# Kernel optimization log

Hardware: AMD Instinct MI355X
Metric: run time of the kernel (lower is better)

## Reference

```python
import jax, jax.numpy as jnp
import numpy as np

N_NODES = 50000


def setup_inputs() -> dict:
    key = jax.random.key(0)
    k1, k2, k3, k4, k5, k6 = jax.random.split(key, 6)
    features = jax.random.normal(k1, (N_NODES, 128), dtype=jnp.float32)
    anchor_distances = jax.random.uniform(k2, (N_NODES, 64), dtype=jnp.float32)
    W = jax.random.normal(k3, (192, 128), dtype=jnp.float32) * (1.0 / np.sqrt(192.0))
    b = jax.random.normal(k4, (128,), dtype=jnp.float32) * 0.01
    src = jax.random.randint(k5, (800000,), 0, N_NODES, dtype=jnp.int32)
    dst = jax.random.randint(k6, (800000,), 0, N_NODES, dtype=jnp.int32)
    return {"features": features, "anchor_distances": anchor_distances,
            "W": W, "b": b, "src": src, "dst": dst}


def reference(features, anchor_distances, W, b, src, dst):
    # Linear(in_feats + num_anchors -> hidden) + ReLU
    combined = jnp.concatenate([features, anchor_distances], axis=1)  # [N, 192]
    h = jax.nn.relu(combined @ W + b)                                  # [N, H]
    # copy_u + mean aggregation: mean of h[src] grouped by dst
    msg_sum = jax.ops.segment_sum(h[src], dst, num_segments=N_NODES)  # [N, H]
    deg = jax.ops.segment_sum(jnp.ones_like(dst, dtype=h.dtype), dst,
                              num_segments=N_NODES)                    # [N]
    # DGL mean leaves 0 for isolated nodes; divide by max(deg, 1)
    out = msg_sum / jnp.maximum(deg, 1.0)[:, None]
    return out
```

## Files before the change

### kernel.cpp

```cpp
#include <hip/hip_runtime.h>
#include <hip/hip_bf16.h>


#define N_NODES 50000
#define N_EDGES 800000
#define HID 128
#define FDIM 128
#define ADIM 64
#define KDIM 192

#define BKT_SH 5
#define BKT_NODES 32
#define NBUCKETS ((N_NODES + BKT_NODES - 1) / BKT_NODES)
#define CAP 1024
#define PC_NBLK 256
#define PC_CHUNK ((N_EDGES + PC_NBLK - 1) / PC_NBLK)
#define EPT 13
#define GEMM_NBLK ((N_NODES + 31) / 32)
#define SA_LD 200

typedef __attribute__((ext_vector_type(8))) short short8;
typedef __attribute__((ext_vector_type(4))) float f32x4;
typedef __attribute__((ext_vector_type(4))) unsigned int u32x4;

__device__ inline unsigned short f2bf(float f) {
  unsigned u = __float_as_uint(f);
  u += 0x7FFFu + ((u >> 16) & 1u);
  return (unsigned short)(u >> 16);
}
__device__ inline unsigned pk2bf(float a, float b) {
  return (unsigned)f2bf(a) | ((unsigned)f2bf(b) << 16);
}
__device__ inline float bf2f(unsigned short s) {
  return __uint_as_float(((unsigned)s) << 16);
}

__global__ __launch_bounds__(256) void wbt_kernel(
    const float* __restrict__ W, unsigned short* __restrict__ WbTf,
    int* __restrict__ bcur) {
  if (blockIdx.x == 0) {
    for (int i = threadIdx.x; i < NBUCKETS; i += 256) bcur[i] = 0;
  }
  int idx = blockIdx.x * 256 + threadIdx.x;
  if (idx >= 2 * 4 * 6 * 64 * 8) return;
  int j = idx & 7;
  int lane = (idx >> 3) & 63;
  int frag = idx >> 9;
  int kk = frag % 6, p = frag / 6;
  int wn = p >> 2, nt = p & 3;
  int col = wn * 64 + nt * 16 + (lane & 15);
  int k = kk * 32 + (lane >> 4) * 8 + j;
  WbTf[idx] = f2bf(W[k * HID + col]);
}

#define SMEM_BYTES (32 * SA_LD * 2)
__global__ __launch_bounds__(256) void gemm_pscatter_kernel(
    const float* __restrict__ F, const float* __restrict__ A,
    const unsigned short* __restrict__ WbTf, const float* __restrict__ bias,
    unsigned short* __restrict__ hb,
    const int* __restrict__ src, const int* __restrict__ dst,
    int* __restrict__ bcur, unsigned* __restrict__ edata, int nrows) {
  __shared__ __align__(16) char smem_raw[SMEM_BYTES];

  if (blockIdx.x < PC_NBLK) {
    int* lh = (int*)smem_raw;
    int* lc = lh + NBUCKETS;
    int bp = blockIdx.x;
    for (int i = threadIdx.x; i < NBUCKETS; i += 256) lh[i] = 0;
    __syncthreads();
    int base = bp * PC_CHUNK;
    int end = base + PC_CHUNK; if (end > N_EDGES) end = N_EDGES;
    int rd[EPT], rs[EPT];
#pragma unroll
    for (int k = 0; k < EPT; ++k) {
      int j = base + threadIdx.x + k * 256;
      if (j < end) {
        rd[k] = dst[j];
        rs[k] = src[j];
        atomicAdd(&lh[rd[k] >> BKT_SH], 1);
      } else {
        rd[k] = -1;
      }
    }
    __syncthreads();
    for (int i = threadIdx.x; i < NBUCKETS; i += 256) {
      int c = lh[i];
      lh[i] = c ? atomicAdd(&bcur[i], c) : 0;
      lc[i] = 0;
    }
    __syncthreads();
#pragma unroll
    for (int k = 0; k < EPT; ++k) {
      if (rd[k] >= 0) {
        int bk = rd[k] >> BKT_SH, dl = rd[k] & (BKT_NODES - 1);
        int p = lh[bk] + atomicAdd(&lc[bk], 1);
        if (p < CAP)
          edata[(bk << 10) + p] = (unsigned)rs[k] | ((unsigned)dl << 16);
      }
    }
    return;
  }

  unsigned short* sA = (unsigned short*)smem_raw;
  const int gblk = blockIdx.x - PC_NBLK;
  const int tid = threadIdx.x;
  const int lane = tid & 63;
  const int wave = tid >> 6;
  const int wm = wave >> 1, wn = wave & 1;
  const int l15 = lane & 15, lg = lane >> 4;
  const int blockrow = gblk * 32;

#pragma unroll
  for (int it = 0; it < 4; ++it) {
    int i = tid + it * 256;
    int row = i >> 5, c4 = (i & 31) * 4;
    int crow = blockrow + row; crow = crow < nrows ? crow : (nrows - 1);
    float4 v = *(const float4*)(F + (size_t)crow * FDIM + c4);
    *(uint2*)(sA + row * SA_LD + c4) = make_uint2(pk2bf(v.x, v.y), pk2bf(v.z, v.w));
  }
#pragma unroll
  for (int it = 0; it < 2; ++it) {
    int i = tid + it * 256;
    int row = i >> 4, c4 = (i & 15) * 4;
    int crow = blockrow + row; crow = crow < nrows ? crow : (nrows - 1);
    float4 v = *(const float4*)(A + (size_t)crow * ADIM + c4);
    *(uint2*)(sA + row * SA_LD + FDIM + c4) = make_uint2(pk2bf(v.x, v.y), pk2bf(v.z, v.w));
  }

  short8 Bf[24];
#pragma unroll
  for (int nt = 0; nt < 4; ++nt)
#pragma unroll
    for (int kk = 0; kk < 6; ++kk)
      Bf[nt * 6 + kk] = *(const short8*)(
          WbTf + ((((wn * 4 + nt) * 6 + kk) << 9) + (lane << 3)));

  __syncthreads();

  short8 Af[6];
  const int rowl = wm * 16 + l15;
#pragma unroll
  for (int kk = 0; kk < 6; ++kk)
    Af[kk] = *(const short8*)(sA + rowl * SA_LD + kk * 32 + lg * 8);

  f32x4 acc[4] = {{0,0,0,0},{0,0,0,0},{0,0,0,0},{0,0,0,0}};
#pragma unroll
  for (int nt = 0; nt < 4; ++nt)
#pragma unroll
    for (int kk = 0; kk < 6; ++kk)
      acc[nt] = __builtin_amdgcn_mfma_f32_16x16x32_bf16(
          Af[kk], Bf[nt * 6 + kk], acc[nt], 0, 0, 0);

  const int rowbase = blockrow + wm * 16;
#pragma unroll
  for (int nt = 0; nt < 4; ++nt) {
    int col = wn * 64 + nt * 16 + l15;
    float bv = bias[col];
#pragma unroll
    for (int q = 0; q < 4; ++q) {
      int row = rowbase + lg * 4 + q;
      if (row < nrows) {
        float v = fmaxf(acc[nt][q] + bv, 0.f);
        hb[(size_t)row * HID + col] = f2bf(v);
      }
    }
  }
}

__device__ inline int wave_incl_scan(int v, int lane) {
#pragma unroll
  for (int off = 1; off < 64; off <<= 1) {
    int t = __shfl_up(v, off, 64);
    if (lane >= off) v += t;
  }
  return v;
}

#define EPT_A (CAP / 256)
__global__ __launch_bounds__(256) void bucket_agg_kernel(
    const unsigned short* __restrict__ hb, const int* __restrict__ bcur,
    const unsigned* __restrict__ edata, float* __restrict__ out) {
  int b = blockIdx.x;
  int nbase = b << BKT_SH;
  int nloc = N_NODES - nbase; if (nloc > BKT_NODES) nloc = BKT_NODES;
  int gb = b << 10;
  int cnt = bcur[b]; cnt = cnt < CAP ? cnt : CAP;
  int t = threadIdx.x, lane = t & 63, wave = t >> 6;
  int g = lane >> 4, l16 = lane & 15;

  __shared__ unsigned short ss[CAP];
  __shared__ int loff[BKT_NODES + 1];
  __shared__ int lcnt[BKT_NODES];
  __shared__ int lcur[BKT_NODES];

  unsigned er[EPT_A];
  if (t < BKT_NODES) lcnt[t] = 0;
  __syncthreads();
#pragma unroll
  for (int k = 0; k < EPT_A; ++k) {
    int j = t + k * 256;
    if (j < cnt) {
      er[k] = edata[gb + j];
      atomicAdd(&lcnt[er[k] >> 16], 1);
    } else {
      er[k] = 0xFFFFFFFFu;
    }
  }
  __syncthreads();
  if (wave == 0) {
    int v = (lane < BKT_NODES) ? lcnt[lane] : 0;
    int incl = wave_incl_scan(v, lane);
    if (lane < BKT_NODES) {
      loff[lane + 1] = incl;
      lcur[lane] = incl - v;
    }
    if (lane == 0) loff[0] = 0;
  }
  __syncthreads();
#pragma unroll
  for (int k = 0; k < EPT_A; ++k) {
    if (er[k] != 0xFFFFFFFFu) {
      int p = atomicAdd(&lcur[er[k] >> 16], 1);
      ss[p] = (unsigned short)(er[k] & 0xFFFFu);
    }
  }
  __syncthreads();
  const unsigned short* hbl = hb + l16 * 8;
  for (int n = wave; n < nloc; n += 4) {
    int s0 = loff[n], s1 = loff[n + 1];
    float acc[8] = {0, 0, 0, 0, 0, 0, 0, 0};
    int j = s0 + g;
    for (; j + 12 < s1; j += 16) {
      int e0 = ss[j], e1 = ss[j + 4], e2 = ss[j + 8], e3 = ss[j + 12];
      u32x4 v0 = *(const u32x4*)(hbl + (size_t)e0 * HID);
      u32x4 v1 = *(const u32x4*)(hbl + (size_t)e1 * HID);
      u32x4 v2 = *(const u32x4*)(hbl + (size_t)e2 * HID);
      u32x4 v3 = *(const u32x4*)(hbl + (size_t)e3 * HID);
#pragma unroll
      for (int i = 0; i < 4; ++i) {
        unsigned w0 = v0[i], w1 = v1[i], w2 = v2[i], w3 = v3[i];
        acc[2 * i]     += (bf2f((unsigned short)(w0 & 0xFFFFu))
                         + bf2f((unsigned short)(w1 & 0xFFFFu)))
                        + (bf2f((unsigned short)(w2 & 0xFFFFu))
                         + bf2f((unsigned short)(w3 & 0xFFFFu)));
        acc[2 * i + 1] += (bf2f((unsigned short)(w0 >> 16))
                         + bf2f((unsigned short)(w1 >> 16)))
                        + (bf2f((unsigned short)(w2 >> 16))
                         + bf2f((unsigned short)(w3 >> 16)));
      }
    }
    for (; j < s1; j += 4) {
      int e0 = ss[j];
      u32x4 v0 = *(const u32x4*)(hbl + (size_t)e0 * HID);
#pragma unroll
      for (int i = 0; i < 4; ++i) {
        unsigned w0 = v0[i];
        acc[2 * i]     += bf2f((unsigned short)(w0 & 0xFFFFu));
        acc[2 * i + 1] += bf2f((unsigned short)(w0 >> 16));
      }
    }
#pragma unroll
    for (int i = 0; i < 8; ++i) {
      acc[i] += __shfl_xor(acc[i], 16, 64);
      acc[i] += __shfl_xor(acc[i], 32, 64);
    }
    if (g == 0) {
      int d = s1 - s0;
      float inv = 1.0f / (float)(d > 1 ? d : 1);
      float* po = out + (size_t)(nbase + n) * HID + l16 * 8;
      *(float4*)po       = make_float4(acc[0]*inv, acc[1]*inv, acc[2]*inv, acc[3]*inv);
      *(float4*)(po + 4) = make_float4(acc[4]*inv, acc[5]*inv, acc[6]*inv, acc[7]*inv);
    }
  }
}

extern "C" void kernel_launch(void* const* d_in, const int* in_sizes, int n_in,
                              void* d_out, int out_size, void* d_ws, size_t ws_size,
                              hipStream_t stream) {
  const float* F   = (const float*)d_in[0];
  const float* A   = (const float*)d_in[1];
  const float* W   = (const float*)d_in[2];
  const float* b   = (const float*)d_in[3];
  const int*   src = (const int*)d_in[4];
  const int*   dst = (const int*)d_in[5];
  float* out = (float*)d_out;

  char* ws = (char*)d_ws;
  size_t off = 0;
  auto alloc = [&](size_t bytes) {
    char* p = ws + off;
    off += (bytes + 255) & ~(size_t)255;
    return p;
  };
  unsigned short* hb   = (unsigned short*)alloc((size_t)N_NODES * HID * 2);
  unsigned short* WbTf = (unsigned short*)alloc((size_t)HID * KDIM * 2);
  int* bcur = (int*)alloc((size_t)NBUCKETS * sizeof(int));
  unsigned* edata = (unsigned*)alloc((size_t)NBUCKETS * CAP * sizeof(unsigned));
  (void)ws_size;

  wbt_kernel<<<(KDIM * HID + 255) / 256, 256, 0, stream>>>(W, WbTf, bcur);
  gemm_pscatter_kernel<<<PC_NBLK + GEMM_NBLK, 256, 0, stream>>>(
      F, A, WbTf, b, hb, src, dst, bcur, edata, N_NODES);
  bucket_agg_kernel<<<NBUCKETS, 256, 0, stream>>>(hb, bcur, edata, out);
}
```

Measured before the change: 67.17 us.

## Replace bucketed edge partitioning with per-node global-atomic adjacency slots

Drops the two-level bucket partition (per-block shared histograms, bucket-offset atomics, and the in-kernel shared-memory counting sort in aggregation). Each edge now does one global atomicAdd on its destination's degree and writes its 16-bit source id into a fixed 64-slot per-node array. The edge scatter is merged into every GEMM block, and aggregation reads each node's slots directly, broadcasting indices with shuffles. This adds 800k contended global atomics and uncoalesced 2-byte writes, and silently drops edges beyond 64 per node. It also stores source ids as 16 bits although node ids reach 50000, which is fine only because that is below 65536.

```diff
diff --git a/kernel.cpp b/kernel.cpp
--- a/kernel.cpp
+++ b/kernel.cpp
@@ -9,14 +9,9 @@
 #define ADIM 64
 #define KDIM 192
 
-#define BKT_SH 5
-#define BKT_NODES 32
-#define NBUCKETS ((N_NODES + BKT_NODES - 1) / BKT_NODES)
-#define CAP 1024
-#define PC_NBLK 256
-#define PC_CHUNK ((N_EDGES + PC_NBLK - 1) / PC_NBLK)
-#define EPT 13
+#define DCAP 64
 #define GEMM_NBLK ((N_NODES + 31) / 32)
+#define EDGE_PER_BLK 512
 #define SA_LD 200
 
 typedef __attribute__((ext_vector_type(8))) short short8;
@@ -37,11 +32,9 @@
 
 __global__ __launch_bounds__(256) void wbt_kernel(
     const float* __restrict__ W, unsigned short* __restrict__ WbTf,
-    int* __restrict__ bcur) {
-  if (blockIdx.x == 0) {
-    for (int i = threadIdx.x; i < NBUCKETS; i += 256) bcur[i] = 0;
-  }
+    int* __restrict__ deg) {
   int idx = blockIdx.x * 256 + threadIdx.x;
+  if (idx < N_NODES) deg[idx] = 0;
   if (idx >= 2 * 4 * 6 * 64 * 8) return;
   int j = idx & 7;
   int lane = (idx >> 3) & 63;
@@ -59,56 +52,31 @@
     const unsigned short* __restrict__ WbTf, const float* __restrict__ bias,
     unsigned short* __restrict__ hb,
     const int* __restrict__ src, const int* __restrict__ dst,
-    int* __restrict__ bcur, unsigned* __restrict__ edata, int nrows) {
+    int* __restrict__ deg, unsigned short* __restrict__ edata, int nrows) {
   __shared__ __align__(16) char smem_raw[SMEM_BYTES];
-
-  if (blockIdx.x < PC_NBLK) {
-    int* lh = (int*)smem_raw;
-    int* lc = lh + NBUCKETS;
-    int bp = blockIdx.x;
-    for (int i = threadIdx.x; i < NBUCKETS; i += 256) lh[i] = 0;
-    __syncthreads();
-    int base = bp * PC_CHUNK;
-    int end = base + PC_CHUNK; if (end > N_EDGES) end = N_EDGES;
-    int rd[EPT], rs[EPT];
-#pragma unroll
-    for (int k = 0; k < EPT; ++k) {
-      int j = base + threadIdx.x + k * 256;
-      if (j < end) {
-        rd[k] = dst[j];
-        rs[k] = src[j];
-        atomicAdd(&lh[rd[k] >> BKT_SH], 1);
-      } else {
-        rd[k] = -1;
+  unsigned short* sA = (unsigned short*)smem_raw;
+  const int tid = threadIdx.x;
+
+  {
+    size_t ebase = (size_t)blockIdx.x * EDGE_PER_BLK + tid;
+#pragma unroll
+    for (int k = 0; k < 2; ++k) {
+      size_t e = ebase + (size_t)k * 256;
+      if (e < N_EDGES) {
+        int s = src[e];
+        int dnode = dst[e];
+        int p = atomicAdd(&deg[dnode], 1);
+        if (p < DCAP)
+          edata[(size_t)dnode * DCAP + p] = (unsigned short)s;
       }
     }
-    __syncthreads();
-    for (int i = threadIdx.x; i < NBUCKETS; i += 256) {
-      int c = lh[i];
-      lh[i] = c ? atomicAdd(&bcur[i], c) : 0;
-      lc[i] = 0;
-    }
-    __syncthreads();
-#pragma unroll
-    for (int k = 0; k < EPT; ++k) {
-      if (rd[k] >= 0) {
-        int bk = rd[k] >> BKT_SH, dl = rd[k] & (BKT_NODES - 1);
-        int p = lh[bk] + atomicAdd(&lc[bk], 1);
-        if (p < CAP)
-          edata[(bk << 10) + p] = (unsigned)rs[k] | ((unsigned)dl << 16);
-      }
-    }
-    return;
-  }
-
-  unsigned short* sA = (unsigned short*)smem_raw;
-  const int gblk = blockIdx.x - PC_NBLK;
-  const int tid = threadIdx.x;
+  }
+
   const int lane = tid & 63;
   const int wave = tid >> 6;
   const int wm = wave >> 1, wn = wave & 1;
   const int l15 = lane & 15, lg = lane >> 4;
-  const int blockrow = gblk * 32;
+  const int blockrow = blockIdx.x * 32;
 
 #pragma unroll
   for (int it = 0; it < 4; ++it) {
@@ -167,110 +135,65 @@
   }
 }
 
-__device__ inline int wave_incl_scan(int v, int lane) {
-#pragma unroll
-  for (int off = 1; off < 64; off <<= 1) {
-    int t = __shfl_up(v, off, 64);
-    if (lane >= off) v += t;
-  }
-  return v;
-}
-
-#define EPT_A (CAP / 256)
-__global__ __launch_bounds__(256) void bucket_agg_kernel(
-    const unsigned short* __restrict__ hb, const int* __restrict__ bcur,
-    const unsigned* __restrict__ edata, float* __restrict__ out) {
-  int b = blockIdx.x;
-  int nbase = b << BKT_SH;
-  int nloc = N_NODES - nbase; if (nloc > BKT_NODES) nloc = BKT_NODES;
-  int gb = b << 10;
-  int cnt = bcur[b]; cnt = cnt < CAP ? cnt : CAP;
-  int t = threadIdx.x, lane = t & 63, wave = t >> 6;
-  int g = lane >> 4, l16 = lane & 15;
-
-  __shared__ unsigned short ss[CAP];
-  __shared__ int loff[BKT_NODES + 1];
-  __shared__ int lcnt[BKT_NODES];
-  __shared__ int lcur[BKT_NODES];
-
-  unsigned er[EPT_A];
-  if (t < BKT_NODES) lcnt[t] = 0;
-  __syncthreads();
-#pragma unroll
-  for (int k = 0; k < EPT_A; ++k) {
-    int j = t + k * 256;
-    if (j < cnt) {
-      er[k] = edata[gb + j];
-      atomicAdd(&lcnt[er[k] >> 16], 1);
-    } else {
-      er[k] = 0xFFFFFFFFu;
+__global__ __launch_bounds__(256) void node_agg_kernel(
+    const unsigned short* __restrict__ hb, const int* __restrict__ deg,
+    const unsigned short* __restrict__ edata, float* __restrict__ out) {
+  const int nbase = blockIdx.x * 32;
+  const int t = threadIdx.x, lane = t & 63, wave = t >> 6;
+  const int g = lane >> 4, l16 = lane & 15;
+  const int gg = wave * 4 + g;
+  const int gbase = g * 16;
+  const unsigned short* hbl = hb + l16 * 8;
+
+  for (int nn = gg; nn < 32; nn += 16) {
+    int n = nbase + nn;
+    if (n >= N_NODES) break;
+    int d = deg[n];
+    int dc = d < DCAP ? d : DCAP;
+    float acc[8] = {0, 0, 0, 0, 0, 0, 0, 0};
+    for (int jb = 0; jb < dc; jb += 16) {
+      int rem = dc - jb; if (rem > 16) rem = 16;
+      int ev = (l16 < rem) ? (int)edata[(size_t)n * DCAP + jb + l16] : 0;
+      int j = 0;
+      for (; j + 3 < rem; j += 4) {
+        int e0 = __shfl(ev, gbase + j,     64);
+        int e1 = __shfl(ev, gbase + j + 1, 64);
+        int e2 = __shfl(ev, gbase + j + 2, 64);
+        int e3 = __shfl(ev, gbase + j + 3, 64);
+        u32x4 v0 = *(const u32x4*)(hbl + (size_t)e0 * HID);
+        u32x4 v1 = *(const u32x4*)(hbl + (size_t)e1 * HID);
+        u32x4 v2 = *(const u32x4*)(hbl + (size_t)e2 * HID);
+        u32x4 v3 = *(const u32x4*)(hbl + (size_t)e3 * HID);
+#pragma unroll
+        for (int i = 0; i < 4; ++i) {
+          unsigned w0 = v0[i], w1 = v1[i], w2 = v2[i], w3 = v3[i];
+          acc[2 * i]     += (bf2f((unsigned short)(w0 & 0xFFFFu))
+                           + bf2f((unsigned short)(w1 & 0xFFFFu)))
+                          + (bf2f((unsigned short)(w2 & 0xFFFFu))
+                           + bf2f((unsigned short)(w3 & 0xFFFFu)));
+          acc[2 * i + 1] += (bf2f((unsigned short)(w0 >> 16))
+                           + bf2f((unsigned short)(w1 >> 16)))
+                          + (bf2f((unsigned short)(w2 >> 16))
+                           + bf2f((unsigned short)(w3 >> 16)));
+        }
+      }
+      for (; j < rem; ++j) {
+        int e0 = __shfl(ev, gbase + j, 64);
+        u32x4 v0 = *(const u32x4*)(hbl + (size_t)e0 * HID);
+#pragma unroll
+        for (int i = 0; i < 4; ++i) {
+          unsigned w0 = v0[i];
+          acc[2 * i]     += bf2f((unsigned short)(w0 & 0xFFFFu));
+          acc[2 * i + 1] += bf2f((unsigned short)(w0 >> 16));
+        }
+      }
     }
-  }
-  __syncthreads();
-  if (wave == 0) {
-    int v = (lane < BKT_NODES) ? lcnt[lane] : 0;
-    int incl = wave_incl_scan(v, lane);
-    if (lane < BKT_NODES) {
-      loff[lane + 1] = incl;
-      lcur[lane] = incl - v;
-    }
-    if (lane == 0) loff[0] = 0;
-  }
-  __syncthreads();
-#pragma unroll
-  for (int k = 0; k < EPT_A; ++k) {
-    if (er[k] != 0xFFFFFFFFu) {
-      int p = atomicAdd(&lcur[er[k] >> 16], 1);
-      ss[p] = (unsigned short)(er[k] & 0xFFFFu);
-    }
-  }
-  __syncthreads();
-  const unsigned short* hbl = hb + l16 * 8;
-  for (int n = wave; n < nloc; n += 4) {
-    int s0 = loff[n], s1 = loff[n + 1];
-    float acc[8] = {0, 0, 0, 0, 0, 0, 0, 0};
-    int j = s0 + g;
-    for (; j + 12 < s1; j += 16) {
-      int e0 = ss[j], e1 = ss[j + 4], e2 = ss[j + 8], e3 = ss[j + 12];
-      u32x4 v0 = *(const u32x4*)(hbl + (size_t)e0 * HID);
-      u32x4 v1 = *(const u32x4*)(hbl + (size_t)e1 * HID);
-      u32x4 v2 = *(const u32x4*)(hbl + (size_t)e2 * HID);
-      u32x4 v3 = *(const u32x4*)(hbl + (size_t)e3 * HID);
-#pragma unroll
-      for (int i = 0; i < 4; ++i) {
-        unsigned w0 = v0[i], w1 = v1[i], w2 = v2[i], w3 = v3[i];
-        acc[2 * i]     += (bf2f((unsigned short)(w0 & 0xFFFFu))
-                         + bf2f((unsigned short)(w1 & 0xFFFFu)))
-                        + (bf2f((unsigned short)(w2 & 0xFFFFu))
-                         + bf2f((unsigned short)(w3 & 0xFFFFu)));
-        acc[2 * i + 1] += (bf2f((unsigned short)(w0 >> 16))
-                         + bf2f((unsigned short)(w1 >> 16)))
-                        + (bf2f((unsigned short)(w2 >> 16))
-                         + bf2f((unsigned short)(w3 >> 16)));
-      }
-    }
-    for (; j < s1; j += 4) {
-      int e0 = ss[j];
-      u32x4 v0 = *(const u32x4*)(hbl + (size_t)e0 * HID);
-#pragma unroll
-      for (int i = 0; i < 4; ++i) {
-        unsigned w0 = v0[i];
-        acc[2 * i]     += bf2f((unsigned short)(w0 & 0xFFFFu));
-        acc[2 * i + 1] += bf2f((unsigned short)(w0 >> 16));
-      }
-    }
-#pragma unroll
-    for (int i = 0; i < 8; ++i) {
-      acc[i] += __shfl_xor(acc[i], 16, 64);
-      acc[i] += __shfl_xor(acc[i], 32, 64);
-    }
-    if (g == 0) {
-      int d = s1 - s0;
-      float inv = 1.0f / (float)(d > 1 ? d : 1);
-      float* po = out + (size_t)(nbase + n) * HID + l16 * 8;
-      *(float4*)po       = make_float4(acc[0]*inv, acc[1]*inv, acc[2]*inv, acc[3]*inv);
-      *(float4*)(po + 4) = make_float4(acc[4]*inv, acc[5]*inv, acc[6]*inv, acc[7]*inv);
-    }
+    float inv = 1.0f / (float)(d > 1 ? d : 1);
+    float* po = out + (size_t)n * HID + l16 * 8;
+    f32x4 o0 = {acc[0] * inv, acc[1] * inv, acc[2] * inv, acc[3] * inv};
+    f32x4 o1 = {acc[4] * inv, acc[5] * inv, acc[6] * inv, acc[7] * inv};
+    *(f32x4*)po = o0;
+    *(f32x4*)(po + 4) = o1;
   }
 }
 
@@ -294,12 +217,13 @@
   };
   unsigned short* hb   = (unsigned short*)alloc((size_t)N_NODES * HID * 2);
   unsigned short* WbTf = (unsigned short*)alloc((size_t)HID * KDIM * 2);
-  int* bcur = (int*)alloc((size_t)NBUCKETS * sizeof(int));
-  unsigned* edata = (unsigned*)alloc((size_t)NBUCKETS * CAP * sizeof(unsigned));
+  int* deg = (int*)alloc((size_t)N_NODES * sizeof(int));
+  unsigned short* edata =
+      (unsigned short*)alloc((size_t)N_NODES * DCAP * sizeof(unsigned short));
   (void)ws_size;
 
-  wbt_kernel<<<(KDIM * HID + 255) / 256, 256, 0, stream>>>(W, WbTf, bcur);
-  gemm_pscatter_kernel<<<PC_NBLK + GEMM_NBLK, 256, 0, stream>>>(
-      F, A, WbTf, b, hb, src, dst, bcur, edata, N_NODES);
-  bucket_agg_kernel<<<NBUCKETS, 256, 0, stream>>>(hb, bcur, edata, out);
-}
+  wbt_kernel<<<(N_NODES + 255) / 256, 256, 0, stream>>>(W, WbTf, deg);
+  gemm_pscatter_kernel<<<GEMM_NBLK, 256, 0, stream>>>(
+      F, A, WbTf, b, hb, src, dst, deg, edata, N_NODES);
+  node_agg_kernel<<<GEMM_NBLK, 256, 0, stream>>>(hb, deg, edata, out);
+}
```

Result: slower. 97.72 us (+45.5%).

## Process two 32-row tiles per GEMM block, reusing weight fragments

Applied to the files above, without the earlier changes.

Each GEMM block now covers 64 rows as two 32-row tiles. The weight fragments and bias are loaded into registers once and reused for both tiles. The second tile's staging into the same shared buffer is issued before the first tile's MFMA compute, so its global loads can overlap with that compute. This halves the number of GEMM blocks and amortizes the weight loads, but it adds extra barriers and exposes less parallelism across the grid.

```diff
diff --git a/kernel.cpp b/kernel.cpp
--- a/kernel.cpp
+++ b/kernel.cpp
@@ -16,7 +16,7 @@
 #define PC_NBLK 256
 #define PC_CHUNK ((N_EDGES + PC_NBLK - 1) / PC_NBLK)
 #define EPT 13
-#define GEMM_NBLK ((N_NODES + 31) / 32)
+#define GEMM_NBLK ((N_NODES + 63) / 64)
 #define SA_LD 200
 
 typedef __attribute__((ext_vector_type(8))) short short8;
@@ -108,24 +108,29 @@
   const int wave = tid >> 6;
   const int wm = wave >> 1, wn = wave & 1;
   const int l15 = lane & 15, lg = lane >> 4;
-  const int blockrow = gblk * 32;
-
-#pragma unroll
-  for (int it = 0; it < 4; ++it) {
-    int i = tid + it * 256;
-    int row = i >> 5, c4 = (i & 31) * 4;
-    int crow = blockrow + row; crow = crow < nrows ? crow : (nrows - 1);
-    float4 v = *(const float4*)(F + (size_t)crow * FDIM + c4);
-    *(uint2*)(sA + row * SA_LD + c4) = make_uint2(pk2bf(v.x, v.y), pk2bf(v.z, v.w));
-  }
-#pragma unroll
-  for (int it = 0; it < 2; ++it) {
-    int i = tid + it * 256;
-    int row = i >> 4, c4 = (i & 15) * 4;
-    int crow = blockrow + row; crow = crow < nrows ? crow : (nrows - 1);
-    float4 v = *(const float4*)(A + (size_t)crow * ADIM + c4);
-    *(uint2*)(sA + row * SA_LD + FDIM + c4) = make_uint2(pk2bf(v.x, v.y), pk2bf(v.z, v.w));
-  }
+  const int br0 = gblk * 64;
+  const int br1 = br0 + 32;
+
+  auto stage = [&](int rowbase) {
+#pragma unroll
+    for (int it = 0; it < 4; ++it) {
+      int i = tid + it * 256;
+      int row = i >> 5, c4 = (i & 31) * 4;
+      int crow = rowbase + row; crow = crow < nrows ? crow : (nrows - 1);
+      float4 v = *(const float4*)(F + (size_t)crow * FDIM + c4);
+      *(uint2*)(sA + row * SA_LD + c4) = make_uint2(pk2bf(v.x, v.y), pk2bf(v.z, v.w));
+    }
+#pragma unroll
+    for (int it = 0; it < 2; ++it) {
+      int i = tid + it * 256;
+      int row = i >> 4, c4 = (i & 15) * 4;
+      int crow = rowbase + row; crow = crow < nrows ? crow : (nrows - 1);
+      float4 v = *(const float4*)(A + (size_t)crow * ADIM + c4);
+      *(uint2*)(sA + row * SA_LD + FDIM + c4) = make_uint2(pk2bf(v.x, v.y), pk2bf(v.z, v.w));
+    }
+  };
+
+  stage(br0);
 
   short8 Bf[24];
 #pragma unroll
@@ -135,35 +140,56 @@
       Bf[nt * 6 + kk] = *(const short8*)(
           WbTf + ((((wn * 4 + nt) * 6 + kk) << 9) + (lane << 3)));
 
-  __syncthreads();
-
+  float bv[4];
+#pragma unroll
+  for (int nt = 0; nt < 4; ++nt) bv[nt] = bias[wn * 64 + nt * 16 + l15];
+
+  __syncthreads();
+
+  const int rowl = wm * 16 + l15;
   short8 Af[6];
-  const int rowl = wm * 16 + l15;
 #pragma unroll
   for (int kk = 0; kk < 6; ++kk)
     Af[kk] = *(const short8*)(sA + rowl * SA_LD + kk * 32 + lg * 8);
 
-  f32x4 acc[4] = {{0,0,0,0},{0,0,0,0},{0,0,0,0},{0,0,0,0}};
-#pragma unroll
-  for (int nt = 0; nt < 4; ++nt)
+  const bool has2 = (br1 < nrows);
+  if (has2) {
+    __syncthreads();
+    stage(br1);
+  }
+
+  auto compute_store = [&](const short8* Afp, int rowbase) {
+    f32x4 acc[4] = {{0,0,0,0},{0,0,0,0},{0,0,0,0},{0,0,0,0}};
+#pragma unroll
+    for (int nt = 0; nt < 4; ++nt)
+#pragma unroll
+      for (int kk = 0; kk < 6; ++kk)
+        acc[nt] = __builtin_amdgcn_mfma_f32_16x16x32_bf16(
+            Afp[kk], Bf[nt * 6 + kk], acc[nt], 0, 0, 0);
+    const int rb = rowbase + wm * 16;
+#pragma unroll
+    for (int nt = 0; nt < 4; ++nt) {
+      int col = wn * 64 + nt * 16 + l15;
+#pragma unroll
+      for (int q = 0; q < 4; ++q) {
+        int row = rb + lg * 4 + q;
+        if (row < nrows) {
+          float v = fmaxf(acc[nt][q] + bv[nt], 0.f);
+          hb[(size_t)row * HID + col] = f2bf(v);
+        }
+      }
+    }
+  };
+
+  compute_store(Af, br0);
+
+  if (has2) {
+    __syncthreads();
+    short8 Af1[6];
 #pragma unroll
     for (int kk = 0; kk < 6; ++kk)
-      acc[nt] = __builtin_amdgcn_mfma_f32_16x16x32_bf16(
-          Af[kk], Bf[nt * 6 + kk], acc[nt], 0, 0, 0);
-
-  const int rowbase = blockrow + wm * 16;
-#pragma unroll
-  for (int nt = 0; nt < 4; ++nt) {
-    int col = wn * 64 + nt * 16 + l15;
-    float bv = bias[col];
-#pragma unroll
-    for (int q = 0; q < 4; ++q) {
-      int row = rowbase + lg * 4 + q;
-      if (row < nrows) {
-        float v = fmaxf(acc[nt][q] + bv, 0.f);
-        hb[(size_t)row * HID + col] = f2bf(v);
-      }
-    }
+      Af1[kk] = *(const short8*)(sA + rowl * SA_LD + kk * 32 + lg * 8);
+    compute_store(Af1, br1);
   }
 }
 
```

Result: faster. 65.36 us (-2.7%).
